# Kernel tuning notes

Measured on AMD Instinct MI355X. Metric: run time of the kernel, lower is better.

Reference implementation:

```python
import jax, jax.numpy as jnp
import numpy as np

K = 11            # involution kernel size
GC = 16           # involution group channels
EPS = 1e-5        # BatchNorm eps


def bn(x, g, b, m, v):
    # eval-mode BatchNorm2d with running stats
    inv = g / jnp.sqrt(v + EPS)
    return x * inv[None, :, None, None] + (b - m * inv)[None, :, None, None]


def conv1x1(x, w, b=None):
    y = jnp.einsum('bchw,oc->bohw', x, w)
    if b is not None:
        y = y + b[None, :, None, None]
    return y


def setup_inputs() -> dict:
    key = jax.random.key(0)
    ks = jax.random.split(key, 32)
    C = 128          # inplanes == planes
    Cm = C // 2      # 64, involution channels
    Mid = Cm // 4    # 16, involution reduce channels
    G = Cm // GC     # 4 groups
    SE = C // 16     # 8
    B, H, W = 1, 160, 160
    f32 = jnp.float32
    rn = lambda k, shape, s=0.05: (jax.random.normal(k, shape, dtype=f32) * s)
    pv = lambda k, n: jax.random.uniform(k, (n,), dtype=f32, minval=0.5, maxval=1.5)
    return {
        'x': jax.random.normal(ks[0], (B, C, H, W), dtype=f32),
        'g1': pv(ks[1], C), 'b1': rn(ks[2], (C,)), 'm1': rn(ks[3], (C,), 0.1), 'v1': pv(ks[4], C),
        'w1': rn(ks[5], (Cm, C)),
        'g2': pv(ks[6], Cm), 'b2': rn(ks[7], (Cm,)), 'm2': rn(ks[8], (Cm,), 0.1), 'v2': pv(ks[9], Cm),
        'inv_w1': rn(ks[10], (Mid, Cm)),
        'ig': pv(ks[11], Mid), 'ib': rn(ks[12], (Mid,)), 'im': rn(ks[13], (Mid,), 0.1), 'iv': pv(ks[14], Mid),
        'inv_w2': rn(ks[15], (K * K * G, Mid)), 'inv_b2': rn(ks[16], (K * K * G,)),
        'g3': pv(ks[17], Cm), 'b3': rn(ks[18], (Cm,)), 'm3': rn(ks[19], (Cm,), 0.1), 'v3': pv(ks[20], Cm),
        'w3': rn(ks[21], (C, Cm)),
        'se_w1': rn(ks[22], (SE, C)), 'se_b1': rn(ks[23], (SE,)),
        'se_w2': rn(ks[24], (C, SE)), 'se_b2': rn(ks[25], (C,)),
    }


def reference(x, g1, b1, m1, v1, w1, g2, b2, m2, v2,
              inv_w1, ig, ib, im, iv, inv_w2, inv_b2,
              g3, b3, m3, v3, w3, se_w1, se_b1, se_w2, se_b2):
    identity = x
    out = jax.nn.elu(bn(x, g1, b1, m1, v1))
    out = conv1x1(out, w1)                              # (B, Cm, H, W)
    out = jax.nn.elu(bn(out, g2, b2, m2, v2))

    # ----- involution(channels=Cm, kernel=11, stride=1) -----
    B, Cm, H, W = out.shape
    G = Cm // GC
    t = jax.nn.relu(bn(conv1x1(out, inv_w1), ig, ib, im, iv))
    wk = conv1x1(t, inv_w2, inv_b2)                     # (B, G*K*K, H, W)
    wk = wk.reshape(B, G, K * K, H, W)
    p = K // 2
    # patches channel order: [C, kh, kw] -> matches torch unfold
    patches = jax.lax.conv_general_dilated_patches(
        out, (K, K), (1, 1), ((p, p), (p, p)))         # (B, Cm*K*K, H, W)
    patches = patches.reshape(B, G, GC, K * K, H, W)
    out = jnp.einsum('bgkhw,bgckhw->bgchw', wk, patches).reshape(B, Cm, H, W)
    # ---------------------------------------------------------

    out = jax.nn.elu(bn(out, g3, b3, m3, v3))
    out = conv1x1(out, w3)                              # (B, C, H, W)

    # SE module
    s = out.mean(axis=(2, 3), keepdims=True)            # (B, C, 1, 1)
    s = jax.nn.relu(conv1x1(s, se_w1, se_b1))
    s = jax.nn.sigmoid(conv1x1(s, se_w2, se_b2))
    return out * s + identity
```

## Files before the change

kernel.cpp:

```cpp
#include <hip/hip_runtime.h>
#include <math.h>

#define HPIX 160
#define WPIX 160
#define NPIX 25600
#define C0   128
#define CM   64
#define MID  16
#define KK   11
#define KK2  121
#define PAD  5
#define PADW 176
#define PADH 170
#define CHP  (PADH*PADW)
#define NBX  (NPIX/256)
#define BN_EPS 1e-5f

__device__ __forceinline__ float elu_f(float y) { return y > 0.f ? y : expm1f(y); }

__global__ __launch_bounds__(256) void k_act(
        const float* __restrict__ x,
        const float* __restrict__ g1, const float* __restrict__ b1,
        const float* __restrict__ m1, const float* __restrict__ v1,
        float* __restrict__ act) {
    int i4 = blockIdx.x * 256 + threadIdx.x;
    int c = i4 / (NPIX / 4);
    float inv  = g1[c] * rsqrtf(v1[c] + BN_EPS);
    float beta = b1[c] - m1[c] * inv;
    float4 xv = ((const float4*)x)[i4];
    float4 o;
    o.x = elu_f(fmaf(xv.x, inv, beta));
    o.y = elu_f(fmaf(xv.y, inv, beta));
    o.z = elu_f(fmaf(xv.z, inv, beta));
    o.w = elu_f(fmaf(xv.w, inv, beta));
    ((float4*)act)[i4] = o;
}

__global__ __launch_bounds__(256, 4) void k_conv1(
        const float* __restrict__ act, const float* __restrict__ w1,
        const float* __restrict__ g2, const float* __restrict__ b2,
        const float* __restrict__ m2, const float* __restrict__ v2,
        float* __restrict__ feat_pad) {
    const int tid = threadIdx.x;
    const int p   = blockIdx.x * 256 + tid;
    const int oc0 = blockIdx.y * 16;
    const float* wbase = w1 + oc0 * C0;

    float acc[16] = {0,0,0,0,0,0,0,0,0,0,0,0,0,0,0,0};
    #pragma unroll 4
    for (int k = 0; k < C0; ++k) {
        float a = act[k * NPIX + p];
        #pragma unroll
        for (int j = 0; j < 16; ++j)
            acc[j] = fmaf(wbase[j * C0 + k], a, acc[j]);
    }

    const int h = p / WPIX, w = p % WPIX;
    const int off = (h + PAD) * PADW + (w + PAD);
    #pragma unroll
    for (int j = 0; j < 16; ++j) {
        int c = oc0 + j;
        float inv = g2[c] * rsqrtf(v2[c] + BN_EPS);
        float y = acc[j] * inv + (b2[c] - m2[c] * inv);
        feat_pad[c * CHP + off] = elu_f(y);
    }
}

__global__ __launch_bounds__(256, 4) void k_conv_t(
        const float* __restrict__ feat_pad, const float* __restrict__ wt,
        const float* __restrict__ g, const float* __restrict__ b,
        const float* __restrict__ m, const float* __restrict__ v,
        float* __restrict__ t) {
    const int tid = threadIdx.x;
    const int p   = blockIdx.x * 256 + tid;
    const int oc0 = blockIdx.y * 4;
    const int h = p / WPIX, w = p % WPIX;
    const int off = (h + PAD) * PADW + (w + PAD);

    float acc[4] = {0,0,0,0};
    #pragma unroll 8
    for (int k = 0; k < CM; ++k) {
        float a = feat_pad[k * CHP + off];
        #pragma unroll
        for (int j = 0; j < 4; ++j)
            acc[j] = fmaf(wt[(oc0 + j) * CM + k], a, acc[j]);
    }
    #pragma unroll
    for (int j = 0; j < 4; ++j) {
        int c = oc0 + j;
        float inv = g[c] * rsqrtf(v[c] + BN_EPS);
        t[c * NPIX + p] = fmaxf(acc[j] * inv + (b[c] - m[c] * inv), 0.f);
    }
}

__global__ __launch_bounds__(256, 4) void k_involution(
        const float* __restrict__ t, const float* __restrict__ feat_pad,
        const float* __restrict__ inv_w2, const float* __restrict__ inv_b2,
        const float* __restrict__ g3, const float* __restrict__ b3,
        const float* __restrict__ m3, const float* __restrict__ v3,
        float* __restrict__ out) {
    __shared__ float s_wk[4 * 66 * 16];
    __shared__ float s_t[MID * 16];

    const int q   = gridDim.x >> 3;
    const int b   = blockIdx.x;
    const int bid = (b & 7) * q + (b >> 3);

    const int tid = threadIdx.x;
    const int p0  = bid * 16;
    const int px  = tid & 15;
    const int jb  = tid >> 4;

    if (tid < MID * 16) s_t[tid] = t[(tid >> 4) * NPIX + p0 + px];
    __syncthreads();

    const float tr0  = s_t[0*16+px],  tr1  = s_t[1*16+px];
    const float tr2  = s_t[2*16+px],  tr3  = s_t[3*16+px];
    const float tr4  = s_t[4*16+px],  tr5  = s_t[5*16+px];
    const float tr6  = s_t[6*16+px],  tr7  = s_t[7*16+px];
    const float tr8  = s_t[8*16+px],  tr9  = s_t[9*16+px];
    const float tr10 = s_t[10*16+px], tr11 = s_t[11*16+px];
    const float tr12 = s_t[12*16+px], tr13 = s_t[13*16+px];
    const float tr14 = s_t[14*16+px], tr15 = s_t[15*16+px];

#define WK_DOT(JSRC, DST) { \
    const float4* wrow_ = (const float4*)(inv_w2 + (JSRC) * MID); \
    float4 w0_ = wrow_[0], w1_ = wrow_[1], w2_ = wrow_[2], w3_ = wrow_[3]; \
    float lo_ = inv_b2[JSRC], hi_ = 0.f; \
    lo_ = fmaf(w0_.x, tr0,  lo_); lo_ = fmaf(w0_.y, tr1,  lo_); \
    lo_ = fmaf(w0_.z, tr2,  lo_); lo_ = fmaf(w0_.w, tr3,  lo_); \
    lo_ = fmaf(w1_.x, tr4,  lo_); lo_ = fmaf(w1_.y, tr5,  lo_); \
    lo_ = fmaf(w1_.z, tr6,  lo_); lo_ = fmaf(w1_.w, tr7,  lo_); \
    hi_ = fmaf(w2_.x, tr8,  hi_); hi_ = fmaf(w2_.y, tr9,  hi_); \
    hi_ = fmaf(w2_.z, tr10, hi_); hi_ = fmaf(w2_.w, tr11, hi_); \
    hi_ = fmaf(w3_.x, tr12, hi_); hi_ = fmaf(w3_.y, tr13, hi_); \
    hi_ = fmaf(w3_.z, tr14, hi_); hi_ = fmaf(w3_.w, tr15, hi_); \
    s_wk[(DST) * 16 + px] = lo_ + hi_; }

    const int tx = tid & 3;
    const int c  = tid >> 2;
    const int g  = c >> 4;
    const int h  = p0 / WPIX;
    const int wb = (p0 % WPIX) + tx * 4;
    const float* fbase = feat_pad + c * CHP + h * PADW + wb;

    float acc0 = 0.f, acc1 = 0.f, acc2 = 0.f, acc3 = 0.f;

    #pragma unroll
    for (int gg = 0; gg < 4; ++gg)
        for (int jl = jb; jl < 55; jl += 16)
            WK_DOT(gg * 121 + jl, gg * 55 + jl);
    __syncthreads();

    #pragma unroll 2
    for (int kh = 0; kh < 5; ++kh) {
        const float4* fp = (const float4*)(fbase + kh * PADW);
        float4 A = fp[0], B = fp[1], Cq = fp[2], D = fp[3];
        float f[16] = {A.x,A.y,A.z,A.w, B.x,B.y,B.z,B.w,
                       Cq.x,Cq.y,Cq.z,Cq.w, D.x,D.y,D.z,D.w};
        const float* wr = s_wk + (g * 55 + kh * 11) * 16 + tx * 4;
        #pragma unroll
        for (int kw = 0; kw < KK; ++kw) {
            float4 wv = *(const float4*)(wr + kw * 16);
            acc0 = fmaf(wv.x, f[kw + 0], acc0);
            acc1 = fmaf(wv.y, f[kw + 1], acc1);
            acc2 = fmaf(wv.z, f[kw + 2], acc2);
            acc3 = fmaf(wv.w, f[kw + 3], acc3);
        }
    }
    __syncthreads();

    #pragma unroll
    for (int gg = 0; gg < 4; ++gg)
        for (int jl = jb; jl < 66; jl += 16)
            WK_DOT(gg * 121 + 55 + jl, gg * 66 + jl);
    __syncthreads();

    #pragma unroll 2
    for (int kh = 5; kh < 11; ++kh) {
        const float4* fp = (const float4*)(fbase + kh * PADW);
        float4 A = fp[0], B = fp[1], Cq = fp[2], D = fp[3];
        float f[16] = {A.x,A.y,A.z,A.w, B.x,B.y,B.z,B.w,
                       Cq.x,Cq.y,Cq.z,Cq.w, D.x,D.y,D.z,D.w};
        const float* wr = s_wk + (g * 66 + (kh - 5) * 11) * 16 + tx * 4;
        #pragma unroll
        for (int kw = 0; kw < KK; ++kw) {
            float4 wv = *(const float4*)(wr + kw * 16);
            acc0 = fmaf(wv.x, f[kw + 0], acc0);
            acc1 = fmaf(wv.y, f[kw + 1], acc1);
            acc2 = fmaf(wv.z, f[kw + 2], acc2);
            acc3 = fmaf(wv.w, f[kw + 3], acc3);
        }
    }
#undef WK_DOT

    float inv  = g3[c] * rsqrtf(v3[c] + BN_EPS);
    float beta = b3[c] - m3[c] * inv;
    float4 o;
    o.x = elu_f(fmaf(acc0, inv, beta));
    o.y = elu_f(fmaf(acc1, inv, beta));
    o.z = elu_f(fmaf(acc2, inv, beta));
    o.w = elu_f(fmaf(acc3, inv, beta));
    *(float4*)(out + c * NPIX + p0 + tx * 4) = o;
}

__global__ __launch_bounds__(256, 4) void k_conv3(
        const float* __restrict__ in, const float* __restrict__ w,
        float* __restrict__ out, float* __restrict__ parts) {
    const int tid = threadIdx.x;
    const int p   = blockIdx.x * 256 + tid;
    const int oc0 = blockIdx.y * 16;
    const float* wbase = w + oc0 * CM;

    float acc[16] = {0,0,0,0,0,0,0,0,0,0,0,0,0,0,0,0};
    #pragma unroll 4
    for (int k = 0; k < CM; ++k) {
        float a = in[k * NPIX + p];
        #pragma unroll
        for (int j = 0; j < 16; ++j)
            acc[j] = fmaf(wbase[j * CM + k], a, acc[j]);
    }
    #pragma unroll
    for (int j = 0; j < 16; ++j)
        out[(oc0 + j) * NPIX + p] = acc[j];

    __shared__ float s_red[16][4];
    const int lane = tid & 63, wid = tid >> 6;
    #pragma unroll
    for (int j = 0; j < 16; ++j) {
        float s = acc[j];
        #pragma unroll
        for (int off = 32; off; off >>= 1) s += __shfl_down(s, off);
        if (lane == 0) s_red[j][wid] = s;
    }
    __syncthreads();
    if (tid < 16) {
        float s = s_red[tid][0] + s_red[tid][1] + s_red[tid][2] + s_red[tid][3];
        parts[(oc0 + tid) * NBX + blockIdx.x] = s;
    }
}

__global__ void k_se(const float* __restrict__ parts,
                     const float* __restrict__ w1, const float* __restrict__ b1,
                     const float* __restrict__ w2, const float* __restrict__ b2,
                     float* __restrict__ scale) {
    __shared__ float s_p[C0];
    __shared__ float s_h[8];
    int tid = threadIdx.x;
    float s = 0.f;
    for (int i = 0; i < NBX; ++i) s += parts[tid * NBX + i];
    s_p[tid] = s * (1.f / NPIX);
    __syncthreads();
    if (tid < 8) {
        float acc = b1[tid];
        for (int c = 0; c < C0; ++c) acc = fmaf(w1[tid * C0 + c], s_p[c], acc);
        s_h[tid] = fmaxf(acc, 0.f);
    }
    __syncthreads();
    float acc = b2[tid];
    #pragma unroll
    for (int j = 0; j < 8; ++j) acc = fmaf(w2[tid * 8 + j], s_h[j], acc);
    scale[tid] = 1.f / (1.f + expf(-acc));
}

__global__ __launch_bounds__(256) void k_final(
        const float* __restrict__ pre, const float* __restrict__ scale,
        const float* __restrict__ x, float* __restrict__ out) {
    int i4 = blockIdx.x * 256 + threadIdx.x;
    int c = i4 / (NPIX / 4);
    float sc = scale[c];
    float4 pv = ((const float4*)pre)[i4];
    float4 xv = ((const float4*)x)[i4];
    float4 o;
    o.x = fmaf(pv.x, sc, xv.x);
    o.y = fmaf(pv.y, sc, xv.y);
    o.z = fmaf(pv.z, sc, xv.z);
    o.w = fmaf(pv.w, sc, xv.w);
    ((float4*)out)[i4] = o;
}

extern "C" void kernel_launch(void* const* d_in, const int* in_sizes, int n_in,
                              void* d_out, int out_size, void* d_ws, size_t ws_size,
                              hipStream_t stream) {
    const float* x      = (const float*)d_in[0];
    const float* g1     = (const float*)d_in[1];
    const float* b1     = (const float*)d_in[2];
    const float* m1     = (const float*)d_in[3];
    const float* v1     = (const float*)d_in[4];
    const float* w1     = (const float*)d_in[5];
    const float* g2     = (const float*)d_in[6];
    const float* b2     = (const float*)d_in[7];
    const float* m2     = (const float*)d_in[8];
    const float* v2     = (const float*)d_in[9];
    const float* inv_w1 = (const float*)d_in[10];
    const float* ig     = (const float*)d_in[11];
    const float* ib     = (const float*)d_in[12];
    const float* im     = (const float*)d_in[13];
    const float* iv     = (const float*)d_in[14];
    const float* inv_w2 = (const float*)d_in[15];
    const float* inv_b2 = (const float*)d_in[16];
    const float* g3     = (const float*)d_in[17];
    const float* b3     = (const float*)d_in[18];
    const float* m3     = (const float*)d_in[19];
    const float* v3     = (const float*)d_in[20];
    const float* w3     = (const float*)d_in[21];
    const float* se_w1  = (const float*)d_in[22];
    const float* se_b1  = (const float*)d_in[23];
    const float* se_w2  = (const float*)d_in[24];
    const float* se_b2  = (const float*)d_in[25];
    float* out = (float*)d_out;

    float* ws       = (float*)d_ws;
    float* act      = ws;
    float* feat_pad = act + C0 * NPIX;
    float* buf_t    = feat_pad + CM * CHP;
    float* buf5     = act;
    float* buf6     = buf_t + MID * NPIX;
    float* parts    = feat_pad;
    float* scale    = buf6 + C0 * NPIX;

    hipMemsetAsync(feat_pad, 0, (size_t)CM * CHP * sizeof(float), stream);

    k_act<<<(C0 * NPIX / 4) / 256, 256, 0, stream>>>(x, g1, b1, m1, v1, act);

    k_conv1<<<dim3(NBX, CM / 16), 256, 0, stream>>>(
        act, w1, g2, b2, m2, v2, feat_pad);

    k_conv_t<<<dim3(NBX, MID / 4), 256, 0, stream>>>(
        feat_pad, inv_w1, ig, ib, im, iv, buf_t);

    k_involution<<<NPIX / 16, 256, 0, stream>>>(buf_t, feat_pad, inv_w2, inv_b2,
                                                g3, b3, m3, v3, buf5);

    k_conv3<<<dim3(NBX, C0 / 16), 256, 0, stream>>>(buf5, w3, buf6, parts);

    k_se<<<1, C0, 0, stream>>>(parts, se_w1, se_b1, se_w2, se_b2, scale);

    k_final<<<(C0 * NPIX / 4) / 256, 256, 0, stream>>>(buf6, scale, x, out);
}
```

Baseline: 127.5 us.

## Double-buffer involution kernel weights to overlap generation with accumulation

The involution kernel now builds its per-pixel kernel weights in four chunks of kernel rows, alternating between two shared-memory buffers. Each chunk is generated while the previous chunk is consumed by the accumulation loop, so a single barrier separates stages instead of two serialized phases. This aims to hide the weight-generation latency behind the FMA work and keeps shared memory about the same size. In exchange there are more barriers (four versus three) and more code, which may raise register pressure.

Measured after the change: 126.8 us. No clear change (-0.6%).

```diff
diff --git a/kernel.cpp b/kernel.cpp
--- a/kernel.cpp
+++ b/kernel.cpp
@@ -99,7 +99,7 @@
         const float* __restrict__ g3, const float* __restrict__ b3,
         const float* __restrict__ m3, const float* __restrict__ v3,
         float* __restrict__ out) {
-    __shared__ float s_wk[4 * 66 * 16];
+    __shared__ float s_wk[2 * 33 * 4 * 16];
     __shared__ float s_t[MID * 16];
 
     const int q   = gridDim.x >> 3;
@@ -123,7 +123,7 @@
     const float tr12 = s_t[12*16+px], tr13 = s_t[13*16+px];
     const float tr14 = s_t[14*16+px], tr15 = s_t[15*16+px];
 
-#define WK_DOT(JSRC, DST) { \
+#define WK_DOT(JSRC, SBUF, DSTJ) { \
     const float4* wrow_ = (const float4*)(inv_w2 + (JSRC) * MID); \
     float4 w0_ = wrow_[0], w1_ = wrow_[1], w2_ = wrow_[2], w3_ = wrow_[3]; \
     float lo_ = inv_b2[JSRC], hi_ = 0.f; \
@@ -135,7 +135,31 @@
     hi_ = fmaf(w2_.z, tr10, hi_); hi_ = fmaf(w2_.w, tr11, hi_); \
     hi_ = fmaf(w3_.x, tr12, hi_); hi_ = fmaf(w3_.y, tr13, hi_); \
     hi_ = fmaf(w3_.z, tr14, hi_); hi_ = fmaf(w3_.w, tr15, hi_); \
-    s_wk[(DST) * 16 + px] = lo_ + hi_; }
+    (SBUF)[(DSTJ) * 16 + px] = lo_ + hi_; }
+
+#define P2_CHUNK(J0, NJ, SBUF) \
+    _Pragma("unroll") \
+    for (int gg = 0; gg < 4; ++gg) \
+        for (int jl = jb; jl < (NJ); jl += 16) \
+            WK_DOT(gg * 121 + (J0) + jl, SBUF, gg * (NJ) + jl)
+
+#define P3_CHUNK(KH0, NKH, NJ, SBUF) \
+    _Pragma("unroll 2") \
+    for (int kh = 0; kh < (NKH); ++kh) { \
+        const float4* fp = (const float4*)(fbase + ((KH0) + kh) * PADW); \
+        float4 A = fp[0], B = fp[1], Cq = fp[2], D = fp[3]; \
+        float f[16] = {A.x,A.y,A.z,A.w, B.x,B.y,B.z,B.w, \
+                       Cq.x,Cq.y,Cq.z,Cq.w, D.x,D.y,D.z,D.w}; \
+        const float* wr = (SBUF) + (g * (NJ) + kh * 11) * 16 + tx * 4; \
+        _Pragma("unroll") \
+        for (int kw = 0; kw < KK; ++kw) { \
+            float4 wv = *(const float4*)(wr + kw * 16); \
+            acc0 = fmaf(wv.x, f[kw + 0], acc0); \
+            acc1 = fmaf(wv.y, f[kw + 1], acc1); \
+            acc2 = fmaf(wv.z, f[kw + 2], acc2); \
+            acc3 = fmaf(wv.w, f[kw + 3], acc3); \
+        } \
+    }
 
     const int tx = tid & 3;
     const int c  = tid >> 2;
@@ -146,53 +170,28 @@
 
     float acc0 = 0.f, acc1 = 0.f, acc2 = 0.f, acc3 = 0.f;
 
-    #pragma unroll
-    for (int gg = 0; gg < 4; ++gg)
-        for (int jl = jb; jl < 55; jl += 16)
-            WK_DOT(gg * 121 + jl, gg * 55 + jl);
-    __syncthreads();
-
-    #pragma unroll 2
-    for (int kh = 0; kh < 5; ++kh) {
-        const float4* fp = (const float4*)(fbase + kh * PADW);
-        float4 A = fp[0], B = fp[1], Cq = fp[2], D = fp[3];
-        float f[16] = {A.x,A.y,A.z,A.w, B.x,B.y,B.z,B.w,
-                       Cq.x,Cq.y,Cq.z,Cq.w, D.x,D.y,D.z,D.w};
-        const float* wr = s_wk + (g * 55 + kh * 11) * 16 + tx * 4;
-        #pragma unroll
-        for (int kw = 0; kw < KK; ++kw) {
-            float4 wv = *(const float4*)(wr + kw * 16);
-            acc0 = fmaf(wv.x, f[kw + 0], acc0);
-            acc1 = fmaf(wv.y, f[kw + 1], acc1);
-            acc2 = fmaf(wv.z, f[kw + 2], acc2);
-            acc3 = fmaf(wv.w, f[kw + 3], acc3);
-        }
-    }
-    __syncthreads();
-
-    #pragma unroll
-    for (int gg = 0; gg < 4; ++gg)
-        for (int jl = jb; jl < 66; jl += 16)
-            WK_DOT(gg * 121 + 55 + jl, gg * 66 + jl);
-    __syncthreads();
-
-    #pragma unroll 2
-    for (int kh = 5; kh < 11; ++kh) {
-        const float4* fp = (const float4*)(fbase + kh * PADW);
-        float4 A = fp[0], B = fp[1], Cq = fp[2], D = fp[3];
-        float f[16] = {A.x,A.y,A.z,A.w, B.x,B.y,B.z,B.w,
-                       Cq.x,Cq.y,Cq.z,Cq.w, D.x,D.y,D.z,D.w};
-        const float* wr = s_wk + (g * 66 + (kh - 5) * 11) * 16 + tx * 4;
-        #pragma unroll
-        for (int kw = 0; kw < KK; ++kw) {
-            float4 wv = *(const float4*)(wr + kw * 16);
-            acc0 = fmaf(wv.x, f[kw + 0], acc0);
-            acc1 = fmaf(wv.y, f[kw + 1], acc1);
-            acc2 = fmaf(wv.z, f[kw + 2], acc2);
-            acc3 = fmaf(wv.w, f[kw + 3], acc3);
-        }
-    }
+    float* bufA = s_wk;
+    float* bufB = s_wk + 2112;
+
+    P2_CHUNK(0, 33, bufA);
+    __syncthreads();
+
+    P2_CHUNK(33, 33, bufB);
+    P3_CHUNK(0, 3, 33, bufA);
+    __syncthreads();
+
+    P2_CHUNK(66, 33, bufA);
+    P3_CHUNK(3, 3, 33, bufB);
+    __syncthreads();
+
+    P2_CHUNK(99, 22, bufB);
+    P3_CHUNK(6, 3, 33, bufA);
+    __syncthreads();
+
+    P3_CHUNK(9, 2, 22, bufB);
 #undef WK_DOT
+#undef P2_CHUNK
+#undef P3_CHUNK
 
     float inv  = g3[c] * rsqrtf(v3[c] + BN_EPS);
     float beta = b3[c] - m3[c] * inv;
```
